# Optimization experiments

Measured on AMD Instinct MI355X. Metric: run time of the kernel, lower is better.

Reference implementation:

```python
import jax, jax.numpy as jnp
import numpy as np

B, H, S, D = 2, 16, 2048, 64


def setup_inputs() -> dict:
    key = jax.random.key(0)
    kq, kk, kv = jax.random.split(key, 3)
    q = jax.random.normal(kq, (B, H, S, D), dtype=jnp.float32)
    k = jax.random.normal(kk, (B, H, S, D), dtype=jnp.float32)
    v = jax.random.normal(kv, (B, H, S, D), dtype=jnp.float32)
    # True = attend (lower triangular); positions where mask == False get -1e9
    causal_mask = jnp.tril(jnp.ones((S, S), dtype=bool))
    return {"q": q, "k": k, "v": v, "causal_mask": causal_mask}


def reference(q, k, v, causal_mask):
    scale = q.shape[-1] ** 0.5
    # [b,h,s,d] @ [b,h,d,t] -> [b,h,s,t]
    pre_score = jnp.einsum("bhsd,bhtd->bhst", q, k) / scale
    pre_score = jnp.where(causal_mask, pre_score, jnp.float32(-1e9))
    # SafeSoftmax: stable softmax along last dim
    attn = jax.nn.softmax(pre_score, axis=-1)
    return jnp.einsum("bhst,bhtd->bhsd", attn, v)
```

## Files before the change

### kernel.cpp

```cpp
#include <hip/hip_runtime.h>


typedef __attribute__((ext_vector_type(8))) short short8;
typedef __attribute__((ext_vector_type(4))) short short4v;
typedef __attribute__((ext_vector_type(4))) float floatx4;
typedef __attribute__((ext_vector_type(4))) int intx4;

constexpr int S = 2048;
constexpr int D = 64;
constexpr size_t TILE_SH = 8 * 64 * 8;
constexpr size_t TENSOR_SH = 32ull * 32 * TILE_SH;
constexpr size_t WS_NEEDED = 2 * TENSOR_SH * 2;

__device__ inline short f2bf(float x){
    unsigned u = __builtin_bit_cast(unsigned, x);
    unsigned r = u + 0x7FFFu + ((u >> 16) & 1u);
    return (short)(r >> 16);
}
__device__ inline float fast_exp2(float x){ return __builtin_amdgcn_exp2f(x); }
__device__ inline short8 as_s8(intx4 v){ union{intx4 i; short8 s;} u; u.i=v; return u.s; }

__global__ __launch_bounds__(256)
void prepack_kernel(const float* __restrict__ K, const float* __restrict__ V,
                    short* __restrict__ Kf, short* __restrict__ Vf)
{
    const int blk = blockIdx.x;
    const int bh = (blk & 7) * 4 + ((blk >> 3) & 3);
    const int kb = blk >> 5;
    const int tid = threadIdx.x;
    const float* Kb = K + (size_t)bh * S * D + (size_t)kb * 64 * D;
    const float* Vb = V + (size_t)bh * S * D + (size_t)kb * 64 * D;
    short* Kfb = Kf + (size_t)(bh * 32 + kb) * TILE_SH;
    short* Vfb = Vf + (size_t)(bh * 32 + kb) * TILE_SH;
#pragma unroll
    for (int h = 0; h < 2; ++h){
        const int s = tid + h * 256;
        const int f = s >> 6, lane = s & 63;
        const int l16 = lane & 15, quad = lane >> 4;
        {
            const int t = f >> 1, kt = f & 1;
            const float* src = Kb + (size_t)(t*16 + l16) * D + kt*32 + quad*8;
            floatx4 a = *(const floatx4*)src;
            floatx4 b = *(const floatx4*)(src + 4);
            short8 v;
            v[0]=f2bf(a.x); v[1]=f2bf(a.y); v[2]=f2bf(a.z); v[3]=f2bf(a.w);
            v[4]=f2bf(b.x); v[5]=f2bf(b.y); v[6]=f2bf(b.z); v[7]=f2bf(b.w);
            *(short8*)&Kfb[(size_t)s * 8] = v;
        }
        {
            const int c = f >> 2, dt = f & 3;
            const int d = dt*16 + l16, key0 = c*32 + quad*8;
            short8 v;
#pragma unroll
            for (int j = 0; j < 8; ++j)
                v[j] = f2bf(Vb[(size_t)(key0 + j) * D + d]);
            *(short8*)&Vfb[(size_t)s * 8] = v;
        }
    }
}

__global__ __launch_bounds__(256, 3)
void fa_fwd_kernel(const float* __restrict__ Q, const short* __restrict__ Kf,
                   const short* __restrict__ Vf, float* __restrict__ Out)
{
    const int tid  = threadIdx.x;
    const int wave = tid >> 6;
    const int lane = tid & 63;
    const int l16  = lane & 15;
    const int quad = lane >> 4;

    const unsigned ub = blockIdx.x;
    const int i  = (int)(ub >> 3);
    const int bh = (int)(ub & 7u) * 4 + (i & 3);
    const int qt = 31 - (i >> 2);
    const int r0 = qt * 64 + wave * 16;
    const int nkb = qt + 1;

    const float* Qb = Q + (size_t)bh * S * D;
    const short* Kfb = Kf + (size_t)bh * 32 * TILE_SH;
    const short* Vfb = Vf + (size_t)bh * 32 * TILE_SH;
    float* Ob = Out + (size_t)bh * S * D;

    const float qscale = 0.125f * 1.44269504f;

    short8 qa[2];
    {
        const float* qptr = Qb + (size_t)(r0 + l16) * D + quad * 8;
#pragma unroll
        for (int kt = 0; kt < 2; ++kt){
            floatx4 f0 = *(const floatx4*)(qptr + kt*32);
            floatx4 f1 = *(const floatx4*)(qptr + kt*32 + 4);
            short8 v;
            v[0]=f2bf(f0.x*qscale); v[1]=f2bf(f0.y*qscale);
            v[2]=f2bf(f0.z*qscale); v[3]=f2bf(f0.w*qscale);
            v[4]=f2bf(f1.x*qscale); v[5]=f2bf(f1.y*qscale);
            v[6]=f2bf(f1.z*qscale); v[7]=f2bf(f1.w*qscale);
            qa[kt] = v;
        }
    }

    float lsum = 0.0f;
    floatx4 Oacc[4];
#pragma unroll
    for (int dt = 0; dt < 4; ++dt) Oacc[dt] = (floatx4){0.f,0.f,0.f,0.f};

    const size_t lofs = (size_t)lane * 8;
    intx4 kreg[8], vreg[8];
#pragma unroll
    for (int s = 0; s < 8; ++s)
        kreg[s] = *(const intx4*)(Kfb + (size_t)s * 512 + lofs);

#pragma unroll 1
    for (int kb = 0; kb < nkb; ++kb){
        const int n0 = kb * 64;
        const short* vt = Vfb + (size_t)kb * TILE_SH;
#pragma unroll
        for (int s = 0; s < 8; ++s)
            vreg[s] = *(const intx4*)(vt + (size_t)s * 512 + lofs);

        const int lastT = min(3, (r0 + 15 - n0) >> 4);

        float p[4][4];
#pragma unroll
        for (int t = 0; t < 4; ++t){
#pragma unroll
            for (int r = 0; r < 4; ++r) p[t][r] = 0.0f;
            if (t > lastT) continue;
            floatx4 acc = (floatx4){0.f,0.f,0.f,0.f};
            acc = __builtin_amdgcn_mfma_f32_16x16x32_bf16(as_s8(kreg[t*2  ]), qa[0], acc, 0,0,0);
            acc = __builtin_amdgcn_mfma_f32_16x16x32_bf16(as_s8(kreg[t*2+1]), qa[1], acc, 0,0,0);
            if (n0 + t*16 + 15 > r0){
                const int keyb = n0 + t*16 + quad*4;
                const int qrow = r0 + l16;
#pragma unroll
                for (int r = 0; r < 4; ++r)
                    acc[r] = (keyb + r <= qrow) ? acc[r] : -1e9f;
            }
#pragma unroll
            for (int r = 0; r < 4; ++r) p[t][r] = acc[r];
        }

        {
            const short* ktn = Kfb + (size_t)(kb + 1 < nkb ? kb + 1 : 0) * TILE_SH;
#pragma unroll
            for (int s = 0; s < 8; ++s)
                kreg[s] = *(const intx4*)(ktn + (size_t)s * 512 + lofs);
        }

#pragma unroll
        for (int t = 0; t < 4; ++t){
            if (t > lastT) continue;
#pragma unroll
            for (int r = 0; r < 4; ++r){
                const float e = fast_exp2(p[t][r]);
                p[t][r] = e;
                lsum += e;
            }
        }

        unsigned pk[4][2];
#pragma unroll
        for (int t = 0; t < 4; ++t)
#pragma unroll
            for (int h = 0; h < 2; ++h){
                unsigned lo = __builtin_bit_cast(unsigned, p[t][2*h]);
                unsigned hi = __builtin_bit_cast(unsigned, p[t][2*h+1]);
                pk[t][h] = (lo >> 16) | (hi & 0xFFFF0000u);
            }

        const int addr_lo = (l16 + ((quad & 1) << 5)) << 2;
        const int addr_hi = addr_lo + 64;
        const bool hiQ = quad >= 2;
#pragma unroll
        for (int c = 0; c < 2; ++c){
            if (2*c > lastT) continue;
            const int ta = 2*c, tb = 2*c + 1;
            int a0 = __builtin_amdgcn_ds_bpermute(addr_lo, (int)pk[ta][0]);
            int b0 = __builtin_amdgcn_ds_bpermute(addr_lo, (int)pk[tb][0]);
            int a1 = __builtin_amdgcn_ds_bpermute(addr_lo, (int)pk[ta][1]);
            int b1 = __builtin_amdgcn_ds_bpermute(addr_lo, (int)pk[tb][1]);
            int a2 = __builtin_amdgcn_ds_bpermute(addr_hi, (int)pk[ta][0]);
            int b2 = __builtin_amdgcn_ds_bpermute(addr_hi, (int)pk[tb][0]);
            int a3 = __builtin_amdgcn_ds_bpermute(addr_hi, (int)pk[ta][1]);
            int b3 = __builtin_amdgcn_ds_bpermute(addr_hi, (int)pk[tb][1]);
            union { intx4 i4; short8 s8; } bf;
            bf.i4[0] = hiQ ? b0 : a0;
            bf.i4[1] = hiQ ? b1 : a1;
            bf.i4[2] = hiQ ? b2 : a2;
            bf.i4[3] = hiQ ? b3 : a3;
#pragma unroll
            for (int dt = 0; dt < 4; ++dt)
                Oacc[dt] = __builtin_amdgcn_mfma_f32_16x16x32_bf16(
                    as_s8(vreg[c*4 + dt]), bf.s8, Oacc[dt], 0,0,0);
        }
    }

    lsum += __shfl_xor(lsum, 16, 64);
    lsum += __shfl_xor(lsum, 32, 64);

    const float inv = 1.0f / lsum;
    float* op = Ob + (size_t)(r0 + l16) * D + quad * 4;
#pragma unroll
    for (int dt = 0; dt < 4; ++dt){
        floatx4 o;
#pragma unroll
        for (int r = 0; r < 4; ++r) o[r] = Oacc[dt][r] * inv;
        *(floatx4*)(op + dt*16) = o;
    }
}

constexpr int KSTR = 72;
constexpr int VSTR = 72;
__global__ __launch_bounds__(256, 2)
void fa_fwd_fallback(const float* __restrict__ Q, const float* __restrict__ K,
                     const float* __restrict__ V, float* __restrict__ Out)
{
    __shared__ short sK [2][64 * KSTR];
    __shared__ short sVt[2][64 * VSTR];
    const int tid  = threadIdx.x;
    const int wave = tid >> 6;
    const int lane = tid & 63;
    const int l16  = lane & 15;
    const int quad = lane >> 4;
    const unsigned ub = blockIdx.x;
    const int bh = (int)((ub & 7u) * 4u + (ub >> 7));
    const int qp = (int)((ub >> 3) & 15u);
    const float* Qb = Q + (size_t)bh * S * D;
    const float* Kb = K + (size_t)bh * S * D;
    const float* Vb = V + (size_t)bh * S * D;
    float* Ob = Out + (size_t)bh * S * D;
    const float qscale = 0.125f * 1.44269504f;
    const int kr = tid >> 2;
    const int kc = (tid & 3) * 16;
    const int vd0   = (tid & 15) * 4;
    const int vkey0 = (tid >> 4) * 4;
    const float* kSrc = Kb + (size_t)kr * D + kc;
    const float* vSrc = Vb + (size_t)vkey0 * D + vd0;
    floatx4 kpre[4], vpre[4];
#pragma unroll
    for (int i = 0; i < 4; ++i) kpre[i] = *(const floatx4*)(kSrc + i*4);
#pragma unroll
    for (int r = 0; r < 4; ++r) vpre[r] = *(const floatx4*)(vSrc + (size_t)r*D);
    int pb = 0;
#pragma unroll 1
    for (int seg = 0; seg < 2; ++seg){
        const int qt  = seg ? (31 - qp) : qp;
        const int nkb = qt + 1;
        const int r0  = qt * 64 + wave * 16;
        short8 qa[2];
        {
            const float* qptr = Qb + (size_t)(r0 + l16) * D + quad * 8;
#pragma unroll
            for (int kt = 0; kt < 2; ++kt){
                floatx4 f0 = *(const floatx4*)(qptr + kt*32);
                floatx4 f1 = *(const floatx4*)(qptr + kt*32 + 4);
                short8 v;
                v[0]=f2bf(f0.x*qscale); v[1]=f2bf(f0.y*qscale);
                v[2]=f2bf(f0.z*qscale); v[3]=f2bf(f0.w*qscale);
                v[4]=f2bf(f1.x*qscale); v[5]=f2bf(f1.y*qscale);
                v[6]=f2bf(f1.z*qscale); v[7]=f2bf(f1.w*qscale);
                qa[kt] = v;
            }
        }
        float mrow = -1e30f, lsum = 0.0f;
        floatx4 Oacc[4];
#pragma unroll
        for (int dt = 0; dt < 4; ++dt) Oacc[dt] = (floatx4){0.f,0.f,0.f,0.f};
#pragma unroll 1
        for (int kb = 0; kb < nkb; ++kb){
            const int n0 = kb * 64;
            {
                short8 w0, w1;
                w0[0]=f2bf(kpre[0].x); w0[1]=f2bf(kpre[0].y); w0[2]=f2bf(kpre[0].z); w0[3]=f2bf(kpre[0].w);
                w0[4]=f2bf(kpre[1].x); w0[5]=f2bf(kpre[1].y); w0[6]=f2bf(kpre[1].z); w0[7]=f2bf(kpre[1].w);
                w1[0]=f2bf(kpre[2].x); w1[1]=f2bf(kpre[2].y); w1[2]=f2bf(kpre[2].z); w1[3]=f2bf(kpre[2].w);
                w1[4]=f2bf(kpre[3].x); w1[5]=f2bf(kpre[3].y); w1[6]=f2bf(kpre[3].z); w1[7]=f2bf(kpre[3].w);
                *(short8*)&sK[pb][kr * KSTR + kc]     = w0;
                *(short8*)&sK[pb][kr * KSTR + kc + 8] = w1;
#pragma unroll
                for (int j = 0; j < 4; ++j){
                    short4v sj;
                    sj[0]=f2bf(vpre[0][j]); sj[1]=f2bf(vpre[1][j]);
                    sj[2]=f2bf(vpre[2][j]); sj[3]=f2bf(vpre[3][j]);
                    *(short4v*)&sVt[pb][(vd0 + j) * VSTR + vkey0] = sj;
                }
            }
            {
                const int n0n = (kb + 1 < nkb) ? (n0 + 64) : 0;
                const float* ks = kSrc + (size_t)n0n * D;
                const float* vs = vSrc + (size_t)n0n * D;
#pragma unroll
                for (int i = 0; i < 4; ++i) kpre[i] = *(const floatx4*)(ks + i*4);
#pragma unroll
                for (int r = 0; r < 4; ++r) vpre[r] = *(const floatx4*)(vs + (size_t)r*D);
            }
            __syncthreads();
            const int lastT = min(3, (r0 + 15 - n0) >> 4);
            float p[4][4];
            float mx = -1e30f;
#pragma unroll
            for (int t = 0; t < 4; ++t){
#pragma unroll
                for (int r = 0; r < 4; ++r) p[t][r] = 0.0f;
                if (t > lastT) continue;
                const short8 kf0 = *(const short8*)&sK[pb][(t*16 + l16) * KSTR + quad*8];
                const short8 kf1 = *(const short8*)&sK[pb][(t*16 + l16) * KSTR + 32 + quad*8];
                floatx4 acc = (floatx4){0.f,0.f,0.f,0.f};
                acc = __builtin_amdgcn_mfma_f32_16x16x32_bf16(kf0, qa[0], acc, 0,0,0);
                acc = __builtin_amdgcn_mfma_f32_16x16x32_bf16(kf1, qa[1], acc, 0,0,0);
                if (n0 + t*16 + 15 > r0){
                    const int keyb = n0 + t*16 + quad*4;
                    const int qrow = r0 + l16;
#pragma unroll
                    for (int r = 0; r < 4; ++r)
                        acc[r] = (keyb + r <= qrow) ? acc[r] : -1e9f;
                }
#pragma unroll
                for (int r = 0; r < 4; ++r){ p[t][r] = acc[r]; mx = fmaxf(mx, acc[r]); }
            }
            mx = fmaxf(mx, __shfl_xor(mx, 16, 64));
            mx = fmaxf(mx, __shfl_xor(mx, 32, 64));
            const float mn = fmaxf(mrow, mx);
            const float al = fast_exp2(mrow - mn);
            mrow = mn;
            float rs = 0.0f;
#pragma unroll
            for (int t = 0; t < 4; ++t){
                if (t > lastT) continue;
#pragma unroll
                for (int r = 0; r < 4; ++r){
                    p[t][r] = fast_exp2(p[t][r] - mn);
                    rs += p[t][r];
                }
            }
            rs += __shfl_xor(rs, 16, 64);
            rs += __shfl_xor(rs, 32, 64);
            lsum = lsum * al + rs;
#pragma unroll
            for (int dt = 0; dt < 4; ++dt)
#pragma unroll
                for (int r = 0; r < 4; ++r) Oacc[dt][r] *= al;
            unsigned pk[4][2];
#pragma unroll
            for (int t = 0; t < 4; ++t)
#pragma unroll
                for (int h = 0; h < 2; ++h){
                    unsigned lo = __builtin_bit_cast(unsigned, p[t][2*h]);
                    unsigned hi = __builtin_bit_cast(unsigned, p[t][2*h+1]);
                    pk[t][h] = (lo >> 16) | (hi & 0xFFFF0000u);
                }
            const int addr_lo = (l16 + ((quad & 1) << 5)) << 2;
            const int addr_hi = addr_lo + 64;
            const bool hiQ = quad >= 2;
#pragma unroll
            for (int c = 0; c < 2; ++c){
                if (2*c > lastT) continue;
                const int ta = 2*c, tb = 2*c + 1;
                int a0 = __builtin_amdgcn_ds_bpermute(addr_lo, (int)pk[ta][0]);
                int b0 = __builtin_amdgcn_ds_bpermute(addr_lo, (int)pk[tb][0]);
                int a1 = __builtin_amdgcn_ds_bpermute(addr_lo, (int)pk[ta][1]);
                int b1 = __builtin_amdgcn_ds_bpermute(addr_lo, (int)pk[tb][1]);
                int a2 = __builtin_amdgcn_ds_bpermute(addr_hi, (int)pk[ta][0]);
                int b2 = __builtin_amdgcn_ds_bpermute(addr_hi, (int)pk[tb][0]);
                int a3 = __builtin_amdgcn_ds_bpermute(addr_hi, (int)pk[ta][1]);
                int b3 = __builtin_amdgcn_ds_bpermute(addr_hi, (int)pk[tb][1]);
                union { intx4 i4; short8 s8; } bf;
                bf.i4[0] = hiQ ? b0 : a0;
                bf.i4[1] = hiQ ? b1 : a1;
                bf.i4[2] = hiQ ? b2 : a2;
                bf.i4[3] = hiQ ? b3 : a3;
#pragma unroll
                for (int dt = 0; dt < 4; ++dt){
                    const short8 vf = *(const short8*)&sVt[pb][(dt*16 + l16) * VSTR + c*32 + quad*8];
                    Oacc[dt] = __builtin_amdgcn_mfma_f32_16x16x32_bf16(vf, bf.s8, Oacc[dt], 0,0,0);
                }
            }
            pb ^= 1;
        }
        const float inv = 1.0f / lsum;
        float* op = Ob + (size_t)(r0 + l16) * D + quad * 4;
#pragma unroll
        for (int dt = 0; dt < 4; ++dt){
            floatx4 o;
#pragma unroll
            for (int r = 0; r < 4; ++r) o[r] = Oacc[dt][r] * inv;
            *(floatx4*)(op + dt*16) = o;
        }
    }
}

extern "C" void kernel_launch(void* const* d_in, const int* in_sizes, int n_in,
                              void* d_out, int out_size, void* d_ws, size_t ws_size,
                              hipStream_t stream) {
    const float* q = (const float*)d_in[0];
    const float* k = (const float*)d_in[1];
    const float* v = (const float*)d_in[2];
    float* out = (float*)d_out;
    if (ws_size >= WS_NEEDED){
        short* Kf = (short*)d_ws;
        short* Vf = Kf + TENSOR_SH;
        hipLaunchKernelGGL(prepack_kernel, dim3(1024), dim3(256), 0, stream, k, v, Kf, Vf);
        hipLaunchKernelGGL(fa_fwd_kernel, dim3(1024), dim3(256), 0, stream, q, Kf, Vf, out);
    } else {
        hipLaunchKernelGGL(fa_fwd_fallback, dim3(512), dim3(256), 0, stream, q, k, v, out);
    }
}
```

Measured before the change: 147.6 us.

## Halve attention block size to 32 query rows and stage V transpose via LDS

The prepack kernel now loads V rows with coalesced vector reads into a padded LDS tile and transposes from shared memory, instead of doing strided scalar global reads. The attention kernel now uses 128-thread blocks covering 32 query rows each, with twice as many blocks, for finer-grained work and better load balance across the causal triangle. The cost is that each key/value tile is reloaded by twice as many blocks, and any shared-memory or sync code in the hidden body must still be correct with two waves.

```diff
diff --git a/kernel.cpp b/kernel.cpp
--- a/kernel.cpp
+++ b/kernel.cpp
@@ -20,10 +20,12 @@
 __device__ inline float fast_exp2(float x){ return __builtin_amdgcn_exp2f(x); }
 __device__ inline short8 as_s8(intx4 v){ union{intx4 i; short8 s;} u; u.i=v; return u.s; }
 
+constexpr int PVSTR = 72;
 __global__ __launch_bounds__(256)
 void prepack_kernel(const float* __restrict__ K, const float* __restrict__ V,
                     short* __restrict__ Kf, short* __restrict__ Vf)
 {
+    __shared__ short sV[64 * PVSTR];
     const int blk = blockIdx.x;
     const int bh = (blk & 7) * 4 + ((blk >> 3) & 3);
     const int kb = blk >> 5;
@@ -32,34 +34,53 @@
     const float* Vb = V + (size_t)bh * S * D + (size_t)kb * 64 * D;
     short* Kfb = Kf + (size_t)(bh * 32 + kb) * TILE_SH;
     short* Vfb = Vf + (size_t)(bh * 32 + kb) * TILE_SH;
+
+    {
+        const int vrow = tid >> 2, vcol = (tid & 3) * 16;
+        const float* src = Vb + (size_t)vrow * D + vcol;
+        floatx4 f0 = *(const floatx4*)(src);
+        floatx4 f1 = *(const floatx4*)(src + 4);
+        floatx4 f2 = *(const floatx4*)(src + 8);
+        floatx4 f3 = *(const floatx4*)(src + 12);
+        short8 w0, w1;
+        w0[0]=f2bf(f0.x); w0[1]=f2bf(f0.y); w0[2]=f2bf(f0.z); w0[3]=f2bf(f0.w);
+        w0[4]=f2bf(f1.x); w0[5]=f2bf(f1.y); w0[6]=f2bf(f1.z); w0[7]=f2bf(f1.w);
+        w1[0]=f2bf(f2.x); w1[1]=f2bf(f2.y); w1[2]=f2bf(f2.z); w1[3]=f2bf(f2.w);
+        w1[4]=f2bf(f3.x); w1[5]=f2bf(f3.y); w1[6]=f2bf(f3.z); w1[7]=f2bf(f3.w);
+        *(short8*)&sV[vrow * PVSTR + vcol]     = w0;
+        *(short8*)&sV[vrow * PVSTR + vcol + 8] = w1;
+    }
 #pragma unroll
     for (int h = 0; h < 2; ++h){
         const int s = tid + h * 256;
         const int f = s >> 6, lane = s & 63;
         const int l16 = lane & 15, quad = lane >> 4;
-        {
-            const int t = f >> 1, kt = f & 1;
-            const float* src = Kb + (size_t)(t*16 + l16) * D + kt*32 + quad*8;
-            floatx4 a = *(const floatx4*)src;
-            floatx4 b = *(const floatx4*)(src + 4);
-            short8 v;
-            v[0]=f2bf(a.x); v[1]=f2bf(a.y); v[2]=f2bf(a.z); v[3]=f2bf(a.w);
-            v[4]=f2bf(b.x); v[5]=f2bf(b.y); v[6]=f2bf(b.z); v[7]=f2bf(b.w);
-            *(short8*)&Kfb[(size_t)s * 8] = v;
-        }
-        {
-            const int c = f >> 2, dt = f & 3;
-            const int d = dt*16 + l16, key0 = c*32 + quad*8;
-            short8 v;
-#pragma unroll
-            for (int j = 0; j < 8; ++j)
-                v[j] = f2bf(Vb[(size_t)(key0 + j) * D + d]);
-            *(short8*)&Vfb[(size_t)s * 8] = v;
-        }
+        const int t = f >> 1, kt = f & 1;
+        const float* src = Kb + (size_t)(t*16 + l16) * D + kt*32 + quad*8;
+        floatx4 a = *(const floatx4*)src;
+        floatx4 b = *(const floatx4*)(src + 4);
+        short8 v;
+        v[0]=f2bf(a.x); v[1]=f2bf(a.y); v[2]=f2bf(a.z); v[3]=f2bf(a.w);
+        v[4]=f2bf(b.x); v[5]=f2bf(b.y); v[6]=f2bf(b.z); v[7]=f2bf(b.w);
+        *(short8*)&Kfb[(size_t)s * 8] = v;
+    }
+    __syncthreads();
+#pragma unroll
+    for (int h = 0; h < 2; ++h){
+        const int s = tid + h * 256;
+        const int f = s >> 6, lane = s & 63;
+        const int l16 = lane & 15, quad = lane >> 4;
+        const int c = f >> 2, dt = f & 3;
+        const int key0 = c*32 + quad*8, d = dt*16 + l16;
+        short8 v;
+#pragma unroll
+        for (int j = 0; j < 8; ++j)
+            v[j] = sV[(key0 + j) * PVSTR + d];
+        *(short8*)&Vfb[(size_t)s * 8] = v;
     }
 }
 
-__global__ __launch_bounds__(256, 3)
+__global__ __launch_bounds__(128, 4)
 void fa_fwd_kernel(const float* __restrict__ Q, const short* __restrict__ Kf,
                    const short* __restrict__ Vf, float* __restrict__ Out)
 {
@@ -70,11 +91,11 @@
     const int quad = lane >> 4;
 
     const unsigned ub = blockIdx.x;
-    const int i  = (int)(ub >> 3);
-    const int bh = (int)(ub & 7u) * 4 + (i & 3);
-    const int qt = 31 - (i >> 2);
-    const int r0 = qt * 64 + wave * 16;
-    const int nkb = qt + 1;
+    const int i   = (int)(ub >> 3);
+    const int bh  = (int)(ub & 7u) * 4 + (i & 3);
+    const int q32 = 63 - (i >> 2);
+    const int r0  = q32 * 32 + wave * 16;
+    const int nkb = (q32 >> 1) + 1;
 
     const float* Qb = Q + (size_t)bh * S * D;
     const short* Kfb = Kf + (size_t)bh * 32 * TILE_SH;
@@ -400,7 +421,7 @@
         short* Kf = (short*)d_ws;
         short* Vf = Kf + TENSOR_SH;
         hipLaunchKernelGGL(prepack_kernel, dim3(1024), dim3(256), 0, stream, k, v, Kf, Vf);
-        hipLaunchKernelGGL(fa_fwd_kernel, dim3(1024), dim3(256), 0, stream, q, Kf, Vf, out);
+        hipLaunchKernelGGL(fa_fwd_kernel, dim3(2048), dim3(128), 0, stream, q, Kf, Vf, out);
     } else {
         hipLaunchKernelGGL(fa_fwd_fallback, dim3(512), dim3(256), 0, stream, q, k, v, out);
     }
```

Result: no change. 147.3 us (-0.2%).
